# Kernel tuning notes

Hardware: AMD Instinct MI355X
Metric: run time of the kernel (lower is better)

Reference implementation:

```python
import jax, jax.numpy as jnp
import numpy as np

N_NODES = 100000
N_EDGES = 1600000
N_FEAT = 64
EXP_FEAT = 50
CUTOFF = 5.0
LOG2 = float(np.log(2.0))


def ssp(x):
    # ShiftedSoftplus: softplus(x) - log(2)
    return jax.nn.softplus(x) - LOG2


def setup_inputs() -> dict:
    key = jax.random.key(0)
    ks = jax.random.split(key, 16)
    s = 1.0 / np.sqrt(N_FEAT)
    se = 1.0 / np.sqrt(EXP_FEAT)
    return {
        "neighbour_index": jax.random.randint(ks[0], (2, N_EDGES), 0, N_NODES, dtype=jnp.int64)
        if jax.config.read("jax_enable_x64") else jax.random.randint(ks[0], (2, N_EDGES), 0, N_NODES, dtype=jnp.int32),
        "neighbour_distances": jax.random.uniform(ks[1], (N_EDGES,), jnp.float32) * CUTOFF,
        "node_features": jax.random.normal(ks[2], (N_NODES, N_FEAT), jnp.float32),
        # initial linear transform
        "lin_w": jax.random.uniform(ks[3], (N_FEAT, N_FEAT), jnp.float32, -s, s),
        "lin_b": jax.random.uniform(ks[4], (N_FEAT,), jnp.float32, -s, s),
        # filter MLP: [EXP_FEAT -> N_FEAT -> N_FEAT], ssp between layers
        "f_w1": jax.random.uniform(ks[5], (N_FEAT, EXP_FEAT), jnp.float32, -se, se),
        "f_b1": jax.random.uniform(ks[6], (N_FEAT,), jnp.float32, -se, se),
        "f_w2": jax.random.uniform(ks[7], (N_FEAT, N_FEAT), jnp.float32, -s, s),
        "f_b2": jax.random.uniform(ks[8], (N_FEAT,), jnp.float32, -s, s),
        # output MLP: [N_FEAT -> N_FEAT -> N_FEAT]
        "m_w1": jax.random.uniform(ks[9], (N_FEAT, N_FEAT), jnp.float32, -s, s),
        "m_b1": jax.random.uniform(ks[10], (N_FEAT,), jnp.float32, -s, s),
        "m_w2": jax.random.uniform(ks[11], (N_FEAT, N_FEAT), jnp.float32, -s, s),
        "m_b2": jax.random.uniform(ks[12], (N_FEAT,), jnp.float32, -s, s),
    }


def reference(neighbour_index, neighbour_distances, node_features,
              lin_w, lin_b, f_w1, f_b1, f_w2, f_b2,
              m_w1, m_b1, m_w2, m_b2):
    n_nodes = node_features.shape[0]
    src = neighbour_index[0]  # j (messages gathered from)
    dst = neighbour_index[1]  # i (messages aggregated into)

    # h_i <- W x_i
    h = node_features @ lin_w.T + lin_b  # [N, F]

    # Gaussian smearing of distances: [E, K]
    centers = jnp.linspace(0.0, CUTOFF, EXP_FEAT, dtype=node_features.dtype)
    delta = centers[1] - centers[0]
    coeff = -0.5 / (delta * delta)
    rbf = jnp.exp(coeff * (neighbour_distances[:, None] - centers[None, :]) ** 2)

    # filter MLP F(r_ij): [E, F]
    filt = ssp(rbf @ f_w1.T + f_b1) @ f_w2.T + f_b2

    # message m_ij = h_j * F(r_ij); scatter-add into targets
    msg = h[src] * filt  # [E, F]
    agg = jax.ops.segment_sum(msg, dst, num_segments=n_nodes)  # [N, F]

    # output MLP
    return ssp(agg @ m_w1.T + m_b1) @ m_w2.T + m_b2
```

## Files before the change

kernel.cpp:

```cpp
#include <hip/hip_runtime.h>
#include <hip/hip_fp16.h>

#define NF 64
#define KEXP 50
#define TBL 2048
#define CUTF 5.0f
#define LOG2C 0.6931471805599453f
#define GRP 64
#define NSC 256
#define GMAX 2048
#define SCAP 1536
#define RPT (SCAP / 256)

typedef unsigned long long ull;
typedef _Float16 f16x8 __attribute__((ext_vector_type(8)));
typedef float f32x4 __attribute__((ext_vector_type(4)));

__device__ __forceinline__ float sspf(float x) {
    return fmaxf(x, 0.0f) + log1pf(expf(-fabsf(x))) - LOG2C;
}

__device__ __forceinline__ f16x8 load_wfrag(const float* __restrict__ w, int f, int k0) {
    const float4 q0 = *(const float4*)(w + (size_t)f * NF + k0);
    const float4 q1 = *(const float4*)(w + (size_t)f * NF + k0 + 4);
    f16x8 r;
    r[0] = (_Float16)q0.x; r[1] = (_Float16)q0.y; r[2] = (_Float16)q0.z; r[3] = (_Float16)q0.w;
    r[4] = (_Float16)q1.x; r[5] = (_Float16)q1.y; r[6] = (_Float16)q1.z; r[7] = (_Float16)q1.w;
    return r;
}

__device__ __forceinline__ f16x8 load_afrag_f32(const float* __restrict__ p) {
    const float4 q0 = *(const float4*)(p);
    const float4 q1 = *(const float4*)(p + 4);
    f16x8 r;
    r[0] = (_Float16)q0.x; r[1] = (_Float16)q0.y; r[2] = (_Float16)q0.z; r[3] = (_Float16)q0.w;
    r[4] = (_Float16)q1.x; r[5] = (_Float16)q1.y; r[6] = (_Float16)q1.z; r[7] = (_Float16)q1.w;
    return r;
}

__global__ void build_tabh2_k(const float* __restrict__ f_w1, const float* __restrict__ f_b1,
                              const float* __restrict__ f_w2, const float* __restrict__ f_b2,
                              __half2* __restrict__ tabh2) {
    __shared__ float rbf_s[KEXP];
    __shared__ float s_s[NF];
    const int t = blockIdx.x;
    const int f = threadIdx.x;
    const float delta = CUTF / (float)(KEXP - 1);
    const float coeff = -0.5f / (delta * delta);
    const float dstep = CUTF / (float)(TBL - 1);
    float vals[2];
    for (int p = 0; p < 2; ++p) {
        const int tt = min(t + p, TBL - 1);
        const float d = (float)tt * dstep;
        __syncthreads();
        if (f < KEXP) {
            float dd = d - (float)f * delta;
            rbf_s[f] = expf(coeff * dd * dd);
        }
        __syncthreads();
        float t1 = f_b1[f];
        for (int k = 0; k < KEXP; ++k) t1 = fmaf(rbf_s[k], f_w1[f * KEXP + k], t1);
        __syncthreads();
        s_s[f] = sspf(t1);
        __syncthreads();
        float t2 = f_b2[f];
        for (int k = 0; k < NF; ++k) t2 = fmaf(s_s[k], f_w2[f * NF + k], t2);
        vals[p] = t2;
    }
    tabh2[(size_t)t * NF + f] =
        __floats2half2_rn(vals[0], (vals[1] - vals[0]) * (1.0f / 256.0f));
}

__global__ void __launch_bounds__(256) prep_k(
    const float* __restrict__ x, const float* __restrict__ w, const float* __restrict__ b,
    __half* __restrict__ h16, int n_nodes)
{
    __shared__ _Float16 stile[4][16][72];
    const int tid = threadIdx.x;
    const int lane = tid & 63;
    const int wid = tid >> 6;
    const int col = lane & 15;
    const int quad = lane >> 4;

    f16x8 bw[4][2];
    float bv[4];
    #pragma unroll
    for (int t = 0; t < 4; ++t) {
        #pragma unroll
        for (int kb = 0; kb < 2; ++kb)
            bw[t][kb] = load_wfrag(w, 16 * t + col, kb * 32 + quad * 8);
        bv[t] = b[16 * t + col];
    }

    const int ntiles = (n_nodes + 15) >> 4;
    for (int tile = blockIdx.x * 4 + wid; tile < ntiles; tile += gridDim.x * 4) {
        const int n0 = tile << 4;
        const int nr = min(n0 + col, n_nodes - 1);
        f16x8 a[2];
        #pragma unroll
        for (int kb = 0; kb < 2; ++kb)
            a[kb] = load_afrag_f32(x + (size_t)nr * NF + kb * 32 + quad * 8);
        f32x4 acc[4];
        #pragma unroll
        for (int t = 0; t < 4; ++t) acc[t] = (f32x4){bv[t], bv[t], bv[t], bv[t]};
        #pragma unroll
        for (int t = 0; t < 4; ++t)
            #pragma unroll
            for (int kb = 0; kb < 2; ++kb)
                acc[t] = __builtin_amdgcn_mfma_f32_16x16x32_f16(a[kb], bw[t][kb], acc[t], 0, 0, 0);
        #pragma unroll
        for (int t = 0; t < 4; ++t)
            #pragma unroll
            for (int r = 0; r < 4; ++r)
                stile[wid][quad * 4 + r][16 * t + col] = (_Float16)acc[t][r];
        __threadfence_block();
        #pragma unroll
        for (int it = 0; it < 2; ++it) {
            const int chunk = it * 64 + lane;
            const int row = chunk >> 3;
            const int off = (chunk & 7) * 8;
            const int n = n0 + row;
            if (n < n_nodes)
                *(uint4*)(h16 + (size_t)n * NF + off) = *(const uint4*)&stile[wid][row][off];
        }
        __threadfence_block();
    }
}

__global__ void __launch_bounds__(1024) hist_k(const int* __restrict__ nbr_dst,
                                               int n_edges, int ngroups, int chk,
                                               unsigned* __restrict__ cnt) {
    __shared__ unsigned cnt_s[GMAX];
    const int tid = threadIdx.x;
    const int c = blockIdx.x;
    const int e0 = c * chk;
    const int e1 = min(e0 + chk, n_edges);
    const int m = max(e1 - e0, 0);
    for (int g = tid; g < ngroups; g += 1024) cnt_s[g] = 0u;
    __syncthreads();
    for (int i = tid; i < m; i += 1024)
        atomicAdd(&cnt_s[(unsigned)nbr_dst[e0 + i] >> 6], 1u);
    __syncthreads();
    const size_t ob = (size_t)c * ngroups;
    for (int g = tid; g < ngroups; g += 1024) cnt[ob + g] = cnt_s[g];
}

__global__ void __launch_bounds__(64) colscan_k(const unsigned* __restrict__ cnt,
                                                unsigned* __restrict__ colpre,
                                                unsigned* __restrict__ tot, int ngroups) {
    const int g = blockIdx.x;
    const int lane = threadIdx.x;
    unsigned v[4];
    unsigned s = 0u;
    #pragma unroll
    for (int j = 0; j < 4; ++j) {
        v[j] = cnt[(size_t)(4 * lane + j) * ngroups + g];
        s += v[j];
    }
    unsigned run = s;
    #pragma unroll
    for (int d = 1; d < 64; d <<= 1) {
        const unsigned t = __shfl_up(run, d, 64);
        if (lane >= d) run += t;
    }
    unsigned pre = run - s;
    #pragma unroll
    for (int j = 0; j < 4; ++j) {
        colpre[(size_t)(4 * lane + j) * ngroups + g] = pre;
        pre += v[j];
    }
    if (lane == 63) tot[g] = run;
}

__global__ void __launch_bounds__(64) base_k(const unsigned* __restrict__ tot,
                                             unsigned* __restrict__ gbase, int ngroups) {
    const int lane = threadIdx.x;
    unsigned carry = 0u;
    for (int base = 0; base < ngroups; base += 64) {
        const int g = base + lane;
        const unsigned v = (g < ngroups) ? tot[g] : 0u;
        unsigned run = v;
        #pragma unroll
        for (int d = 1; d < 64; d <<= 1) {
            const unsigned t = __shfl_up(run, d, 64);
            if (lane >= d) run += t;
        }
        if (g < ngroups) gbase[g] = carry + run - v;
        carry += (unsigned)__shfl((int)run, 63, 64);
    }
    if (lane == 0) gbase[ngroups] = carry;
}

__global__ void __launch_bounds__(1024) scatter2_k(const int* __restrict__ nbr,
                                                   const float* __restrict__ dist,
                                                   int n_edges, int ngroups, int chk,
                                                   const unsigned* __restrict__ colpre,
                                                   const unsigned* __restrict__ gbase,
                                                   ull* __restrict__ payload) {
    __shared__ unsigned cur_s[GMAX];
    const int tid = threadIdx.x;
    const int c = blockIdx.x;
    const int e0 = c * chk;
    const int e1 = min(e0 + chk, n_edges);
    const int m = max(e1 - e0, 0);
    const size_t ob = (size_t)c * ngroups;
    for (int g = tid; g < ngroups; g += 1024) cur_s[g] = gbase[g] + colpre[ob + g];
    __syncthreads();
    const float scale = (float)(TBL - 1) / CUTF;
    for (int i = tid; i < m; i += 1024) {
        const int e = e0 + i;
        const unsigned dst = (unsigned)nbr[n_edges + e];
        const unsigned src = (unsigned)nbr[e];
        const float xx = dist[e] * scale;
        int i0 = (int)xx;
        i0 = max(0, min(i0, TBL - 2));
        const float fr = xx - (float)i0;
        const unsigned fr8 = min((unsigned)(fr * 256.0f), 255u);
        const ull rec = (ull)(((unsigned)i0 << 8) | fr8) |
                        ((ull)((src << 7) | (dst & 63u)) << 32);
        const unsigned pos = atomicAdd(&cur_s[dst >> 6], 1u);
        payload[pos] = rec;
    }
}

__global__ void __launch_bounds__(256) agg_k(
    const ull* __restrict__ payload, const unsigned* __restrict__ gbase,
    const __half* __restrict__ h16, const __half2* __restrict__ tabh2,
    float* __restrict__ agg, int n_nodes)
{
    __shared__ ull sorted_s[SCAP];
    __shared__ unsigned cnt_s[GRP];
    __shared__ unsigned base_s[GRP];
    __shared__ unsigned cur_s[GRP];
    const int tid = threadIdx.x;
    const int lane = tid & 63;
    const int wid = tid >> 6;
    const int g = blockIdx.x;
    const unsigned beg = gbase[g];
    const unsigned end = gbase[g + 1];
    const unsigned tot = min(end - beg, (unsigned)SCAP);

    if (tid < GRP) cnt_s[tid] = 0u;
    __syncthreads();
    ull rec[RPT];
    #pragma unroll
    for (int k = 0; k < RPT; ++k) {
        const unsigned i = (unsigned)(k * 256) + tid;
        rec[k] = 0ull;
        if (i < tot) {
            rec[k] = payload[beg + i];
            atomicAdd(&cnt_s[(unsigned)(rec[k] >> 32) & 63u], 1u);
        }
    }
    __syncthreads();
    if (tid < GRP) {
        const unsigned c = cnt_s[tid];
        unsigned run = c;
        #pragma unroll
        for (int d = 1; d < 64; d <<= 1) {
            const unsigned t = __shfl_up(run, d, 64);
            if (tid >= d) run += t;
        }
        base_s[tid] = run - c;
        cur_s[tid]  = run - c;
    }
    __syncthreads();
    #pragma unroll
    for (int k = 0; k < RPT; ++k) {
        const unsigned i = (unsigned)(k * 256) + tid;
        if (i < tot) {
            const unsigned pos = atomicAdd(&cur_s[(unsigned)(rec[k] >> 32) & 63u], 1u);
            sorted_s[pos] = rec[k];
        }
    }
    __syncthreads();
    const char* tabB = (const char*)tabh2 + (lane << 2);
    const char* hB   = (const char*)h16 + (lane << 1);
    auto ev = [&](ull r) -> float {
        const unsigned lo = (unsigned)r;
        const unsigned hi = (unsigned)(r >> 32);
        const float2 t = __half22float2(*(const __half2*)(tabB + (lo & 0xFFFFFF00u)));
        const float hv = __half2float(*(const __half*)(hB + (hi & 0xFFFFFF80u)));
        return hv * fmaf((float)(lo & 255u), t.y, t.x);
    };
    const int n0 = g * GRP;
    for (int rr = 0; rr < 16; ++rr) {
        const int r = (wid << 4) + rr;
        unsigned i = base_s[r];
        const unsigned e = cur_s[r];
        float acc0 = 0.f, acc1 = 0.f;
        for (; i + 8u <= e; i += 8u) {
            const ull r0 = sorted_s[i];
            const ull r1 = sorted_s[i + 1];
            const ull r2 = sorted_s[i + 2];
            const ull r3 = sorted_s[i + 3];
            const ull r4 = sorted_s[i + 4];
            const ull r5 = sorted_s[i + 5];
            const ull r6 = sorted_s[i + 6];
            const ull r7 = sorted_s[i + 7];
            acc0 += (ev(r0) + ev(r1)) + (ev(r2) + ev(r3));
            acc1 += (ev(r4) + ev(r5)) + (ev(r6) + ev(r7));
        }
        for (; i < e; ++i) acc0 += ev(sorted_s[i]);
        const int n = n0 + r;
        if (n < n_nodes) agg[(size_t)n * NF + lane] = acc0 + acc1;
    }
}

__global__ void __launch_bounds__(64) oflow2_k(const ull* __restrict__ payload,
                                               const unsigned* __restrict__ gbase,
                                               const __half* __restrict__ h16,
                                               const __half2* __restrict__ tabh2,
                                               float* __restrict__ agg) {
    const int g = blockIdx.x;
    const unsigned beg = gbase[g];
    const unsigned end = gbase[g + 1];
    if (end - beg <= (unsigned)SCAP) return;
    const int lane = threadIdx.x;
    const char* tabB = (const char*)tabh2 + (lane << 2);
    const char* hB   = (const char*)h16 + (lane << 1);
    for (unsigned i = beg + SCAP; i < end; ++i) {
        const ull rec = payload[i];
        const unsigned lo = (unsigned)rec;
        const unsigned hi = (unsigned)(rec >> 32);
        const float2 t = __half22float2(*(const __half2*)(tabB + (lo & 0xFFFFFF00u)));
        const float hv = __half2float(*(const __half*)(hB + (hi & 0xFFFFFF80u)));
        const float filt = fmaf((float)(lo & 255u), t.y, t.x);
        const unsigned row = (unsigned)g * GRP + (hi & 63u);
        atomicAdd(agg + (size_t)row * NF + lane, hv * filt);
    }
}

__global__ void edge_k(const int* __restrict__ nbr, const float* __restrict__ dist,
                       const __half* __restrict__ h16, const __half2* __restrict__ tabh2,
                       float* __restrict__ agg, int n_edges) {
    const int tid = threadIdx.x;
    const int lane = tid & 63;
    const int nwaves = (gridDim.x * blockDim.x) >> 6;
    const int gw = (blockIdx.x * blockDim.x + tid) >> 6;
    const float scale = (float)(TBL - 1) / CUTF;
    const int nbatch = n_edges >> 6;
    for (int bb = gw; bb < nbatch; bb += nwaves) {
        const int e0 = bb << 6;
        int src = nbr[e0 + lane];
        int dst = nbr[n_edges + e0 + lane];
        float d = dist[e0 + lane];
        float xx = d * scale;
        int i0 = (int)xx;
        i0 = max(0, min(i0, TBL - 2));
        float frac = xx - (float)i0;
        #pragma unroll 4
        for (int j = 0; j < 64; ++j) {
            const int sj = __shfl(src, j);
            const int dj = __shfl(dst, j);
            const int ij = __shfl(i0, j);
            const float fj = __shfl(frac, j);
            const float2 tv = __half22float2(tabh2[(size_t)ij * NF + lane]);
            const float filt = fmaf(fj * 256.0f, tv.y, tv.x);
            const float hv = __half2float(h16[(size_t)sj * NF + lane]);
            atomicAdd(agg + (size_t)dj * NF + lane, hv * filt);
        }
    }
    if (gw == 0) {
        for (int e = nbatch << 6; e < n_edges; ++e) {
            const int sj = nbr[e];
            const int dj = nbr[n_edges + e];
            const float d = dist[e];
            float xx = d * scale;
            int ij = (int)xx;
            ij = max(0, min(ij, TBL - 2));
            const float fj = xx - (float)ij;
            const float2 tv = __half22float2(tabh2[(size_t)ij * NF + lane]);
            const float filt = fmaf(fj * 256.0f, tv.y, tv.x);
            const float hv = __half2float(h16[(size_t)sj * NF + lane]);
            atomicAdd(agg + (size_t)dj * NF + lane, hv * filt);
        }
    }
}

__global__ void __launch_bounds__(256) out_mlp_k(const float* __restrict__ agg,
                                                 const float* __restrict__ w1,
                                                 const float* __restrict__ b1,
                                                 const float* __restrict__ w2,
                                                 const float* __restrict__ b2,
                                                 float* __restrict__ out, int n_nodes) {
    __shared__ _Float16 stile[4][16][72];
    const int tid = threadIdx.x;
    const int lane = tid & 63;
    const int wid = tid >> 6;
    const int col = lane & 15;
    const int quad = lane >> 4;

    f16x8 bw1[4][2], bw2[4][2];
    float b1v[4], b2v[4];
    #pragma unroll
    for (int t = 0; t < 4; ++t) {
        #pragma unroll
        for (int kb = 0; kb < 2; ++kb) {
            bw1[t][kb] = load_wfrag(w1, 16 * t + col, kb * 32 + quad * 8);
            bw2[t][kb] = load_wfrag(w2, 16 * t + col, kb * 32 + quad * 8);
        }
        b1v[t] = b1[16 * t + col];
        b2v[t] = b2[16 * t + col];
    }

    const int ntiles = (n_nodes + 15) >> 4;
    for (int tile = blockIdx.x * 4 + wid; tile < ntiles; tile += gridDim.x * 4) {
        const int n0 = tile << 4;
        const int nr = min(n0 + col, n_nodes - 1);
        f16x8 a[2];
        #pragma unroll
        for (int kb = 0; kb < 2; ++kb)
            a[kb] = load_afrag_f32(agg + (size_t)nr * NF + kb * 32 + quad * 8);
        f32x4 acc[4];
        #pragma unroll
        for (int t = 0; t < 4; ++t) acc[t] = (f32x4){b1v[t], b1v[t], b1v[t], b1v[t]};
        #pragma unroll
        for (int t = 0; t < 4; ++t)
            #pragma unroll
            for (int kb = 0; kb < 2; ++kb)
                acc[t] = __builtin_amdgcn_mfma_f32_16x16x32_f16(a[kb], bw1[t][kb], acc[t], 0, 0, 0);
        #pragma unroll
        for (int t = 0; t < 4; ++t)
            #pragma unroll
            for (int r = 0; r < 4; ++r)
                stile[wid][quad * 4 + r][16 * t + col] = (_Float16)sspf(acc[t][r]);
        __threadfence_block();
        f16x8 a2[2];
        #pragma unroll
        for (int kb = 0; kb < 2; ++kb)
            a2[kb] = *(const f16x8*)&stile[wid][col][kb * 32 + quad * 8];
        f32x4 acc2[4];
        #pragma unroll
        for (int t = 0; t < 4; ++t) acc2[t] = (f32x4){b2v[t], b2v[t], b2v[t], b2v[t]};
        #pragma unroll
        for (int t = 0; t < 4; ++t)
            #pragma unroll
            for (int kb = 0; kb < 2; ++kb)
                acc2[t] = __builtin_amdgcn_mfma_f32_16x16x32_f16(a2[kb], bw2[t][kb], acc2[t], 0, 0, 0);
        #pragma unroll
        for (int t = 0; t < 4; ++t)
            #pragma unroll
            for (int r = 0; r < 4; ++r) {
                const int n = n0 + quad * 4 + r;
                if (n < n_nodes) out[(size_t)n * NF + 16 * t + col] = acc2[t][r];
            }
        __threadfence_block();
    }
}

extern "C" void kernel_launch(void* const* d_in, const int* in_sizes, int n_in,
                              void* d_out, int out_size, void* d_ws, size_t ws_size,
                              hipStream_t stream) {
    const int*   nbr   = (const int*)d_in[0];
    const float* dist  = (const float*)d_in[1];
    const float* x     = (const float*)d_in[2];
    const float* lin_w = (const float*)d_in[3];
    const float* lin_b = (const float*)d_in[4];
    const float* f_w1  = (const float*)d_in[5];
    const float* f_b1  = (const float*)d_in[6];
    const float* f_w2  = (const float*)d_in[7];
    const float* f_b2  = (const float*)d_in[8];
    const float* m_w1  = (const float*)d_in[9];
    const float* m_b1  = (const float*)d_in[10];
    const float* m_w2  = (const float*)d_in[11];
    const float* m_b2  = (const float*)d_in[12];

    const int n_edges = in_sizes[1];
    const int n_nodes = in_sizes[2] / NF;
    const int ngroups = (n_nodes + GRP - 1) / GRP;
    const int chk     = (n_edges + NSC - 1) / NSC;
    const int ntiles  = (n_nodes + 15) / 16;
    const int mlp_blk = (ntiles + 3) / 4;

    float* out = (float*)d_out;
    float* agg = out;

    char* ws = (char*)d_ws;
    size_t off = 0;
    auto alloc = [&](size_t bytes) { char* p = ws + off; off = (off + bytes + 255) & ~(size_t)255; return p; };
    __half*   h16     = (__half*)alloc((size_t)n_nodes * NF * sizeof(__half));
    __half2*  tabh2   = (__half2*)alloc((size_t)TBL * NF * sizeof(__half2));
    unsigned* cnt     = (unsigned*)alloc((size_t)NSC * ngroups * sizeof(unsigned));
    unsigned* colpre  = (unsigned*)alloc((size_t)NSC * ngroups * sizeof(unsigned));
    unsigned* tot     = (unsigned*)alloc((size_t)ngroups * sizeof(unsigned));
    unsigned* gbase   = (unsigned*)alloc((size_t)(ngroups + 1) * sizeof(unsigned));
    ull*      payload = (ull*)alloc((size_t)NSC * chk * sizeof(ull));
    const bool sort_path = (off <= ws_size) && (ngroups <= GMAX) && (n_nodes <= (1 << 17));

    build_tabh2_k<<<TBL, 64, 0, stream>>>(f_w1, f_b1, f_w2, f_b2, tabh2);
    prep_k<<<mlp_blk, 256, 0, stream>>>(x, lin_w, lin_b, h16, n_nodes);

    if (sort_path) {
        hist_k<<<NSC, 1024, 0, stream>>>(nbr + n_edges, n_edges, ngroups, chk, cnt);
        colscan_k<<<ngroups, 64, 0, stream>>>(cnt, colpre, tot, ngroups);
        base_k<<<1, 64, 0, stream>>>(tot, gbase, ngroups);
        scatter2_k<<<NSC, 1024, 0, stream>>>(nbr, dist, n_edges, ngroups, chk,
                                             colpre, gbase, payload);
        agg_k<<<ngroups, 256, 0, stream>>>(payload, gbase, h16, tabh2, agg, n_nodes);
        oflow2_k<<<ngroups, 64, 0, stream>>>(payload, gbase, h16, tabh2, agg);
    } else {
        hipMemsetAsync(agg, 0, (size_t)n_nodes * NF * sizeof(float), stream);
        edge_k<<<2048, 256, 0, stream>>>(nbr, dist, h16, tabh2, agg, n_edges);
    }
    out_mlp_k<<<mlp_blk, 256, 0, stream>>>(agg, m_w1, m_b1, m_w2, m_b2, out, n_nodes);
}
```

Measured before the change: 208.3 us.

## Replace interpolated filter table with denser nearest-neighbour fp16 table

```diff
diff --git a/kernel.cpp b/kernel.cpp
--- a/kernel.cpp
+++ b/kernel.cpp
@@ -3,11 +3,11 @@
 
 #define NF 64
 #define KEXP 50
-#define TBL 2048
+#define TBL 16384
 #define CUTF 5.0f
 #define LOG2C 0.6931471805599453f
 #define GRP 64
-#define NSC 256
+#define NSC 128
 #define GMAX 2048
 #define SCAP 1536
 #define RPT (SCAP / 256)
@@ -38,37 +38,28 @@
     return r;
 }
 
-__global__ void build_tabh2_k(const float* __restrict__ f_w1, const float* __restrict__ f_b1,
+__global__ void build_tabnn_k(const float* __restrict__ f_w1, const float* __restrict__ f_b1,
                               const float* __restrict__ f_w2, const float* __restrict__ f_b2,
-                              __half2* __restrict__ tabh2) {
+                              __half* __restrict__ tabnn) {
     __shared__ float rbf_s[KEXP];
     __shared__ float s_s[NF];
     const int t = blockIdx.x;
     const int f = threadIdx.x;
     const float delta = CUTF / (float)(KEXP - 1);
     const float coeff = -0.5f / (delta * delta);
-    const float dstep = CUTF / (float)(TBL - 1);
-    float vals[2];
-    for (int p = 0; p < 2; ++p) {
-        const int tt = min(t + p, TBL - 1);
-        const float d = (float)tt * dstep;
-        __syncthreads();
-        if (f < KEXP) {
-            float dd = d - (float)f * delta;
-            rbf_s[f] = expf(coeff * dd * dd);
-        }
-        __syncthreads();
-        float t1 = f_b1[f];
-        for (int k = 0; k < KEXP; ++k) t1 = fmaf(rbf_s[k], f_w1[f * KEXP + k], t1);
-        __syncthreads();
-        s_s[f] = sspf(t1);
-        __syncthreads();
-        float t2 = f_b2[f];
-        for (int k = 0; k < NF; ++k) t2 = fmaf(s_s[k], f_w2[f * NF + k], t2);
-        vals[p] = t2;
-    }
-    tabh2[(size_t)t * NF + f] =
-        __floats2half2_rn(vals[0], (vals[1] - vals[0]) * (1.0f / 256.0f));
+    const float d = (float)t * (CUTF / (float)(TBL - 1));
+    if (f < KEXP) {
+        float dd = d - (float)f * delta;
+        rbf_s[f] = expf(coeff * dd * dd);
+    }
+    __syncthreads();
+    float t1 = f_b1[f];
+    for (int k = 0; k < KEXP; ++k) t1 = fmaf(rbf_s[k], f_w1[f * KEXP + k], t1);
+    s_s[f] = sspf(t1);
+    __syncthreads();
+    float t2 = f_b2[f];
+    for (int k = 0; k < NF; ++k) t2 = fmaf(s_s[k], f_w2[f * NF + k], t2);
+    tabnn[(size_t)t * NF + f] = __float2half(t2);
 }
 
 __global__ void __launch_bounds__(256) prep_k(
@@ -150,25 +141,18 @@
                                                 unsigned* __restrict__ tot, int ngroups) {
     const int g = blockIdx.x;
     const int lane = threadIdx.x;
-    unsigned v[4];
-    unsigned s = 0u;
-    #pragma unroll
-    for (int j = 0; j < 4; ++j) {
-        v[j] = cnt[(size_t)(4 * lane + j) * ngroups + g];
-        s += v[j];
-    }
+    const unsigned a = cnt[(size_t)(2 * lane) * ngroups + g];
+    const unsigned b = cnt[(size_t)(2 * lane + 1) * ngroups + g];
+    const unsigned s = a + b;
     unsigned run = s;
     #pragma unroll
     for (int d = 1; d < 64; d <<= 1) {
         const unsigned t = __shfl_up(run, d, 64);
         if (lane >= d) run += t;
     }
-    unsigned pre = run - s;
-    #pragma unroll
-    for (int j = 0; j < 4; ++j) {
-        colpre[(size_t)(4 * lane + j) * ngroups + g] = pre;
-        pre += v[j];
-    }
+    const unsigned pre = run - s;
+    colpre[(size_t)(2 * lane) * ngroups + g] = pre;
+    colpre[(size_t)(2 * lane + 1) * ngroups + g] = pre + a;
     if (lane == 63) tot[g] = run;
 }
 
@@ -211,12 +195,10 @@
         const int e = e0 + i;
         const unsigned dst = (unsigned)nbr[n_edges + e];
         const unsigned src = (unsigned)nbr[e];
-        const float xx = dist[e] * scale;
+        const float xx = dist[e] * scale + 0.5f;
         int i0 = (int)xx;
-        i0 = max(0, min(i0, TBL - 2));
-        const float fr = xx - (float)i0;
-        const unsigned fr8 = min((unsigned)(fr * 256.0f), 255u);
-        const ull rec = (ull)(((unsigned)i0 << 8) | fr8) |
+        i0 = max(0, min(i0, TBL - 1));
+        const ull rec = (ull)((unsigned)i0 << 7) |
                         ((ull)((src << 7) | (dst & 63u)) << 32);
         const unsigned pos = atomicAdd(&cur_s[dst >> 6], 1u);
         payload[pos] = rec;
@@ -225,7 +207,7 @@
 
 __global__ void __launch_bounds__(256) agg_k(
     const ull* __restrict__ payload, const unsigned* __restrict__ gbase,
-    const __half* __restrict__ h16, const __half2* __restrict__ tabh2,
+    const __half* __restrict__ h16, const __half* __restrict__ tabnn,
     float* __restrict__ agg, int n_nodes)
 {
     __shared__ ull sorted_s[SCAP];
@@ -274,14 +256,14 @@
         }
     }
     __syncthreads();
-    const char* tabB = (const char*)tabh2 + (lane << 2);
+    const char* tabB = (const char*)tabnn + (lane << 1);
     const char* hB   = (const char*)h16 + (lane << 1);
     auto ev = [&](ull r) -> float {
         const unsigned lo = (unsigned)r;
         const unsigned hi = (unsigned)(r >> 32);
-        const float2 t = __half22float2(*(const __half2*)(tabB + (lo & 0xFFFFFF00u)));
+        const float tv = __half2float(*(const __half*)(tabB + lo));
         const float hv = __half2float(*(const __half*)(hB + (hi & 0xFFFFFF80u)));
-        return hv * fmaf((float)(lo & 255u), t.y, t.x);
+        return tv * hv;
     };
     const int n0 = g * GRP;
     for (int rr = 0; rr < 16; ++rr) {
@@ -289,17 +271,23 @@
         unsigned i = base_s[r];
         const unsigned e = cur_s[r];
         float acc0 = 0.f, acc1 = 0.f;
-        for (; i + 8u <= e; i += 8u) {
+        for (; i + 16u <= e; i += 16u) {
+            ull rv[16];
+            #pragma unroll
+            for (int j = 0; j < 16; ++j) rv[j] = sorted_s[i + j];
+            float p[16];
+            #pragma unroll
+            for (int j = 0; j < 16; ++j) p[j] = ev(rv[j]);
+            acc0 += ((p[0] + p[1]) + (p[2] + p[3])) + ((p[4] + p[5]) + (p[6] + p[7]));
+            acc1 += ((p[8] + p[9]) + (p[10] + p[11])) + ((p[12] + p[13]) + (p[14] + p[15]));
+        }
+        for (; i + 4u <= e; i += 4u) {
             const ull r0 = sorted_s[i];
             const ull r1 = sorted_s[i + 1];
             const ull r2 = sorted_s[i + 2];
             const ull r3 = sorted_s[i + 3];
-            const ull r4 = sorted_s[i + 4];
-            const ull r5 = sorted_s[i + 5];
-            const ull r6 = sorted_s[i + 6];
-            const ull r7 = sorted_s[i + 7];
-            acc0 += (ev(r0) + ev(r1)) + (ev(r2) + ev(r3));
-            acc1 += (ev(r4) + ev(r5)) + (ev(r6) + ev(r7));
+            acc0 += ev(r0) + ev(r1);
+            acc1 += ev(r2) + ev(r3);
         }
         for (; i < e; ++i) acc0 += ev(sorted_s[i]);
         const int n = n0 + r;
@@ -310,29 +298,28 @@
 __global__ void __launch_bounds__(64) oflow2_k(const ull* __restrict__ payload,
                                                const unsigned* __restrict__ gbase,
                                                const __half* __restrict__ h16,
-                                               const __half2* __restrict__ tabh2,
+                                               const __half* __restrict__ tabnn,
                                                float* __restrict__ agg) {
     const int g = blockIdx.x;
     const unsigned beg = gbase[g];
     const unsigned end = gbase[g + 1];
     if (end - beg <= (unsigned)SCAP) return;
     const int lane = threadIdx.x;
-    const char* tabB = (const char*)tabh2 + (lane << 2);
+    const char* tabB = (const char*)tabnn + (lane << 1);
     const char* hB   = (const char*)h16 + (lane << 1);
     for (unsigned i = beg + SCAP; i < end; ++i) {
         const ull rec = payload[i];
         const unsigned lo = (unsigned)rec;
         const unsigned hi = (unsigned)(rec >> 32);
-        const float2 t = __half22float2(*(const __half2*)(tabB + (lo & 0xFFFFFF00u)));
+        const float tv = __half2float(*(const __half*)(tabB + lo));
         const float hv = __half2float(*(const __half*)(hB + (hi & 0xFFFFFF80u)));
-        const float filt = fmaf((float)(lo & 255u), t.y, t.x);
         const unsigned row = (unsigned)g * GRP + (hi & 63u);
-        atomicAdd(agg + (size_t)row * NF + lane, hv * filt);
+        atomicAdd(agg + (size_t)row * NF + lane, tv * hv);
     }
 }
 
 __global__ void edge_k(const int* __restrict__ nbr, const float* __restrict__ dist,
-                       const __half* __restrict__ h16, const __half2* __restrict__ tabh2,
+                       const __half* __restrict__ h16, const __half* __restrict__ tabnn,
                        float* __restrict__ agg, int n_edges) {
     const int tid = threadIdx.x;
     const int lane = tid & 63;
@@ -345,20 +332,17 @@
         int src = nbr[e0 + lane];
         int dst = nbr[n_edges + e0 + lane];
         float d = dist[e0 + lane];
-        float xx = d * scale;
+        float xx = d * scale + 0.5f;
         int i0 = (int)xx;
-        i0 = max(0, min(i0, TBL - 2));
-        float frac = xx - (float)i0;
+        i0 = max(0, min(i0, TBL - 1));
         #pragma unroll 4
         for (int j = 0; j < 64; ++j) {
             const int sj = __shfl(src, j);
             const int dj = __shfl(dst, j);
             const int ij = __shfl(i0, j);
-            const float fj = __shfl(frac, j);
-            const float2 tv = __half22float2(tabh2[(size_t)ij * NF + lane]);
-            const float filt = fmaf(fj * 256.0f, tv.y, tv.x);
+            const float tv = __half2float(tabnn[(size_t)ij * NF + lane]);
             const float hv = __half2float(h16[(size_t)sj * NF + lane]);
-            atomicAdd(agg + (size_t)dj * NF + lane, hv * filt);
+            atomicAdd(agg + (size_t)dj * NF + lane, tv * hv);
         }
     }
     if (gw == 0) {
@@ -366,14 +350,12 @@
             const int sj = nbr[e];
             const int dj = nbr[n_edges + e];
             const float d = dist[e];
-            float xx = d * scale;
+            float xx = d * scale + 0.5f;
             int ij = (int)xx;
-            ij = max(0, min(ij, TBL - 2));
-            const float fj = xx - (float)ij;
-            const float2 tv = __half22float2(tabh2[(size_t)ij * NF + lane]);
-            const float filt = fmaf(fj * 256.0f, tv.y, tv.x);
+            ij = max(0, min(ij, TBL - 1));
+            const float tv = __half2float(tabnn[(size_t)ij * NF + lane]);
             const float hv = __half2float(h16[(size_t)sj * NF + lane]);
-            atomicAdd(agg + (size_t)dj * NF + lane, hv * filt);
+            atomicAdd(agg + (size_t)dj * NF + lane, tv * hv);
         }
     }
 }
@@ -480,7 +462,7 @@
     size_t off = 0;
     auto alloc = [&](size_t bytes) { char* p = ws + off; off = (off + bytes + 255) & ~(size_t)255; return p; };
     __half*   h16     = (__half*)alloc((size_t)n_nodes * NF * sizeof(__half));
-    __half2*  tabh2   = (__half2*)alloc((size_t)TBL * NF * sizeof(__half2));
+    __half*   tabnn   = (__half*)alloc((size_t)TBL * NF * sizeof(__half));
     unsigned* cnt     = (unsigned*)alloc((size_t)NSC * ngroups * sizeof(unsigned));
     unsigned* colpre  = (unsigned*)alloc((size_t)NSC * ngroups * sizeof(unsigned));
     unsigned* tot     = (unsigned*)alloc((size_t)ngroups * sizeof(unsigned));
@@ -488,7 +470,7 @@
     ull*      payload = (ull*)alloc((size_t)NSC * chk * sizeof(ull));
     const bool sort_path = (off <= ws_size) && (ngroups <= GMAX) && (n_nodes <= (1 << 17));
 
-    build_tabh2_k<<<TBL, 64, 0, stream>>>(f_w1, f_b1, f_w2, f_b2, tabh2);
+    build_tabnn_k<<<TBL, 64, 0, stream>>>(f_w1, f_b1, f_w2, f_b2, tabnn);
     prep_k<<<mlp_blk, 256, 0, stream>>>(x, lin_w, lin_b, h16, n_nodes);
 
     if (sort_path) {
@@ -497,11 +479,11 @@
         base_k<<<1, 64, 0, stream>>>(tot, gbase, ngroups);
         scatter2_k<<<NSC, 1024, 0, stream>>>(nbr, dist, n_edges, ngroups, chk,
                                              colpre, gbase, payload);
-        agg_k<<<ngroups, 256, 0, stream>>>(payload, gbase, h16, tabh2, agg, n_nodes);
-        oflow2_k<<<ngroups, 64, 0, stream>>>(payload, gbase, h16, tabh2, agg);
+        agg_k<<<ngroups, 256, 0, stream>>>(payload, gbase, h16, tabnn, agg, n_nodes);
+        oflow2_k<<<ngroups, 64, 0, stream>>>(payload, gbase, h16, tabnn, agg);
     } else {
         hipMemsetAsync(agg, 0, (size_t)n_nodes * NF * sizeof(float), stream);
-        edge_k<<<2048, 256, 0, stream>>>(nbr, dist, h16, tabh2, agg, n_edges);
+        edge_k<<<2048, 256, 0, stream>>>(nbr, dist, h16, tabnn, agg, n_edges);
     }
     out_mlp_k<<<mlp_blk, 256, 0, stream>>>(agg, m_w1, m_b1, m_w2, m_b2, out, n_nodes);
 }
```

After: 219.1 us. 5.2% more time.
